# Kernel tuning notes

Measured on AMD Instinct MI355X. Metric: run time of the kernel, lower is better.

Reference implementation:

```python
import jax, jax.numpy as jnp
import numpy as np

B, S, C = 4, 8192, 256        # batch, seq len, channels
NW, WS, PSZ, D = 2048, 256, 256, 32  # words, word_size, p_size, window radius


def setup_inputs() -> dict:
    key = jax.random.key(0)
    k0, k1, k2, k3, k4 = jax.random.split(key, 5)
    q = jax.random.normal(k0, (B, S, C), jnp.float32)
    c_t = jax.random.normal(k1, (B, NW, WS), jnp.float32)
    # scale weights ~1/sqrt(fan_in) so sigmoid in predictive alignment is not saturated
    W_a = jax.random.normal(k2, (WS, C), jnp.float32) / np.sqrt(C).astype(np.float32)
    W_p = jax.random.normal(k3, (PSZ, WS), jnp.float32) / np.sqrt(WS).astype(np.float32)
    V_p = jax.random.normal(k4, (1, PSZ), jnp.float32) / np.sqrt(PSZ).astype(np.float32)
    return {"q": q, "c_t": c_t, "W_a": W_a, "W_p": W_p, "V_p": V_p}


def reference(q, c_t, W_a, W_p, V_p):
    Bq, Sq, Cq = q.shape
    # predictive alignment: p_t = S * sigmoid(V_p(tanh(W_p(c_t))))  -> [B, NW, 1]
    p_t = Sq * jax.nn.sigmoid(jnp.tanh(c_t @ W_p.T) @ V_p.T)
    # window positions s in [p-D, p+D]; torch .long() truncates (p_t > 0 so == floor)
    offs = jnp.arange(-D, D + 1)                       # [K]
    s = p_t[..., 0].astype(jnp.int32)[:, :, None] + offs  # [B, NW, K]
    # pad a leading NaN row; out-of-range indices map to it (clamp then mod)
    q_pad = jnp.concatenate([jnp.full((Bq, 1, Cq), jnp.nan, q.dtype), q], axis=1)  # [B, S+1, C]
    idx = jnp.clip(s + 1, 0, Sq + 1) % (Sq + 1)        # S+1 wraps to the NaN row (0)
    qw = jax.vmap(lambda qb, ib: qb[ib])(q_pad, idx)   # [B, NW, K, C] gathered windows
    nan_mask = jnp.isnan(qw[..., 0])                   # [B, NW, K]
    qw = jnp.where(nan_mask[..., None], 0.0, qw)       # zero invalid keys (used for output too)
    Wq = qw @ W_a.T                                    # [B, NW, K, WS]
    a_t = jnp.einsum('bwkd,bwd->bwk', Wq, c_t)         # per-window scores
    a_t = jnp.where(nan_mask, -jnp.inf, a_t)           # NaN keys -> -inf before softmax
    prob = jax.nn.softmax(a_t, axis=2)
    # Gaussian truncation around predicted position p_t
    prob = prob * jnp.exp(-2.0 * jnp.square((s.astype(q.dtype) - p_t) / D))
    out = jnp.einsum('bwk,bwkc->bwc', prob, qw)        # [B, NW, C]
    return out
```

## Files before the change

### kernel.cpp

```cpp
#include <hip/hip_runtime.h>
#include <math.h>

#define BB 4
#define S 8192
#define C 256
#define NW 2048
#define WS 256
#define PSZ 256
#define DD 32
#define KK 65
#define TOTW (BB * NW)

#define KC 64
#define LDA 68
#define NBKT 64
#define TBKT (BB * NBKT)

__global__ __launch_bounds__(256) void prep_B(const float* __restrict__ Wp,
                                              const float* __restrict__ Wa,
                                              float* __restrict__ Bp,
                                              int* __restrict__ cnt) {
    const int k = blockIdx.x;
    const int t = threadIdx.x;
    Bp[k * 512 + t] = Wp[t * WS + k];
    Bp[k * 512 + 256 + t] = Wa[k * C + t];
    if (k == 0) cnt[t] = 0;
}

__global__ __launch_bounds__(256, 4) void precomp_gemm(const float* __restrict__ ct,
                                                       const float* __restrict__ Bp,
                                                       const float* __restrict__ Vp,
                                                       float* __restrict__ ptpart,
                                                       float* __restrict__ g) {
    __shared__ __align__(16) float Al[KC][LDA];
    __shared__ __align__(16) float Bl[KC][LDA];

    const int t = threadIdx.x;
    const int bm = blockIdx.x >> 3;
    const int bn = blockIdx.x & 7;
    const int tm = t >> 4;
    const int tn = t & 15;
    const int sm = t >> 2;
    const int sf = t & 3;

    const float4* ct4 = (const float4*)ct;
    const float4* B4  = (const float4*)Bp;

    float acc[4][4] = {{0.f}};

    for (int kc = 0; kc < 256; kc += KC) {
        __syncthreads();
#pragma unroll
        for (int i = 0; i < 4; i++) {
            const float4 a = ct4[(size_t)(bm * 64 + sm) * 64 + (kc >> 2) + sf + i * 4];
            const int kl = (sf + i * 4) * 4;
            Al[kl + 0][sm] = a.x;
            Al[kl + 1][sm] = a.y;
            Al[kl + 2][sm] = a.z;
            Al[kl + 3][sm] = a.w;
        }
#pragma unroll
        for (int i = 0; i < 4; i++) {
            const float4 b = B4[(size_t)(kc + sm) * 128 + bn * 16 + sf + i * 4];
            *(float4*)&Bl[sm][(sf + i * 4) * 4] = b;
        }
        __syncthreads();

#pragma unroll 8
        for (int kk = 0; kk < KC; kk++) {
            const float4 a = *(const float4*)&Al[kk][tm * 4];
            const float4 b = *(const float4*)&Bl[kk][tn * 4];
            acc[0][0] = fmaf(a.x, b.x, acc[0][0]);
            acc[0][1] = fmaf(a.x, b.y, acc[0][1]);
            acc[0][2] = fmaf(a.x, b.z, acc[0][2]);
            acc[0][3] = fmaf(a.x, b.w, acc[0][3]);
            acc[1][0] = fmaf(a.y, b.x, acc[1][0]);
            acc[1][1] = fmaf(a.y, b.y, acc[1][1]);
            acc[1][2] = fmaf(a.y, b.z, acc[1][2]);
            acc[1][3] = fmaf(a.y, b.w, acc[1][3]);
            acc[2][0] = fmaf(a.z, b.x, acc[2][0]);
            acc[2][1] = fmaf(a.z, b.y, acc[2][1]);
            acc[2][2] = fmaf(a.z, b.z, acc[2][2]);
            acc[2][3] = fmaf(a.z, b.w, acc[2][3]);
            acc[3][0] = fmaf(a.w, b.x, acc[3][0]);
            acc[3][1] = fmaf(a.w, b.y, acc[3][1]);
            acc[3][2] = fmaf(a.w, b.z, acc[3][2]);
            acc[3][3] = fmaf(a.w, b.w, acc[3][3]);
        }
    }

    if (bn >= 4) {
        const int col = bn * 64 + tn * 4 - 256;
#pragma unroll
        for (int i = 0; i < 4; i++) {
            const int row = bm * 64 + tm * 4 + i;
            *(float4*)&g[(size_t)row * 256 + col] =
                make_float4(acc[i][0], acc[i][1], acc[i][2], acc[i][3]);
        }
    } else {
        const float4 vp4 = ((const float4*)Vp)[bn * 16 + tn];
#pragma unroll
        for (int i = 0; i < 4; i++) {
            float v = tanhf(acc[i][0]) * vp4.x;
            v = fmaf(tanhf(acc[i][1]), vp4.y, v);
            v = fmaf(tanhf(acc[i][2]), vp4.z, v);
            v = fmaf(tanhf(acc[i][3]), vp4.w, v);
#pragma unroll
            for (int off = 8; off >= 1; off >>= 1) v += __shfl_xor(v, off);
            if (tn == 0) {
                const int row = bm * 64 + tm * 4 + i;
                ptpart[row * 4 + bn] = v;
            }
        }
    }
}

__global__ __launch_bounds__(256) void pt_hist(const float* __restrict__ ptpart,
                                               float* __restrict__ pt,
                                               int* __restrict__ cnt) {
    const int wg = blockIdx.x * 256 + threadIdx.x;
    const float4 pp = ((const float4*)ptpart)[wg];
    const float x = (pp.x + pp.y) + (pp.z + pp.w);
    const float p = (float)S / (1.f + expf(-x));
    pt[wg] = p;
    const int s0 = (int)p;
    const int bkt = (wg >> 11) * NBKT + min(NBKT - 1, max(0, s0 >> 7));
    atomicAdd(&cnt[bkt], 1);
}

__global__ __launch_bounds__(256) void scan_kernel(const int* __restrict__ cnt,
                                                   int* __restrict__ offs) {
    __shared__ int sh[TBKT];
    const int t = threadIdx.x;
    const int v = cnt[t];
    sh[t] = v;
    __syncthreads();
    for (int d = 1; d < TBKT; d <<= 1) {
        const int x = (t >= d) ? sh[t - d] : 0;
        __syncthreads();
        sh[t] += x;
        __syncthreads();
    }
    offs[t] = sh[t] - v;
}

__global__ __launch_bounds__(256) void scatter_kernel(const float* __restrict__ pt,
                                                      int* __restrict__ offs,
                                                      int* __restrict__ perm) {
    const int wg = blockIdx.x * 256 + threadIdx.x;
    const int s0 = (int)pt[wg];
    const int bkt = (wg >> 11) * NBKT + min(NBKT - 1, max(0, s0 >> 7));
    const int pos = atomicAdd(&offs[bkt], 1);
    perm[pos] = wg;
}

__global__ __launch_bounds__(256) void attn(const float* __restrict__ q,
                                            const float* __restrict__ g,
                                            const float* __restrict__ pt,
                                            const int* __restrict__ perm,
                                            float* __restrict__ out) {
    const int tid = threadIdx.x;
    const int lane = tid & 63;
    const int wv = tid >> 6;
    const int bid = blockIdx.x;
    const int sb = (bid & 7) * 256 + (bid >> 3);
    const int wg = perm[sb * 4 + wv];
    const int b = wg >> 11;
    const int grp = lane >> 4;
    const int sub = lane & 15;

    const float p = pt[wg];
    const int s0 = (int)p;

    const float* grow = g + (size_t)wg * C + sub * 4;
    const float4 g0 = *(const float4*)(grow);
    const float4 g1 = *(const float4*)(grow + 64);
    const float4 g2 = *(const float4*)(grow + 128);
    const float4 g3 = *(const float4*)(grow + 192);

    const float* qb = q + (size_t)b * S * C + sub * 4;

    float e[17];
#pragma unroll
    for (int it = 0; it < 17; it++) {
        const int k = it * 4 + grp;
        const int s = s0 + k - DD;
        const bool valid = (k <= 64) && ((unsigned)s < (unsigned)S);
        const float* qr = qb + (size_t)min(max(s, 0), S - 1) * C;
        const float4 q0 = *(const float4*)(qr);
        const float4 q1 = *(const float4*)(qr + 64);
        const float4 q2 = *(const float4*)(qr + 128);
        const float4 q3 = *(const float4*)(qr + 192);

        float d0 = q0.x * g0.x, d1 = q1.x * g1.x, d2 = q2.x * g2.x, d3 = q3.x * g3.x;
        d0 = fmaf(q0.y, g0.y, d0); d1 = fmaf(q1.y, g1.y, d1);
        d2 = fmaf(q2.y, g2.y, d2); d3 = fmaf(q3.y, g3.y, d3);
        d0 = fmaf(q0.z, g0.z, d0); d1 = fmaf(q1.z, g1.z, d1);
        d2 = fmaf(q2.z, g2.z, d2); d3 = fmaf(q3.z, g3.z, d3);
        d0 = fmaf(q0.w, g0.w, d0); d1 = fmaf(q1.w, g1.w, d1);
        d2 = fmaf(q2.w, g2.w, d2); d3 = fmaf(q3.w, g3.w, d3);
        float d = (d0 + d1) + (d2 + d3);
#pragma unroll
        for (int off = 8; off >= 1; off >>= 1) d += __shfl_xor(d, off);
        e[it] = valid ? d : -3e38f;
    }

    float m = e[0];
#pragma unroll
    for (int it = 1; it < 17; it++) m = fmaxf(m, e[it]);
    float M = fmaxf(m, __shfl_xor(m, 16));
    M = fmaxf(M, __shfl_xor(M, 32));

    float den = 0.f;
#pragma unroll
    for (int it = 0; it < 17; it++) {
        e[it] = __expf(e[it] - M);
        den += e[it];
    }
    den += __shfl_xor(den, 16);
    den += __shfl_xor(den, 32);

#pragma unroll
    for (int it = 0; it < 17; it++) {
        const int s = s0 + it * 4 + grp - DD;
        const float fs = (float)s - p;
        const float tt = fs * (1.f / (float)DD);
        e[it] *= __expf(-2.f * tt * tt);
    }

    float4 a0 = {0, 0, 0, 0}, a1 = {0, 0, 0, 0}, a2 = {0, 0, 0, 0}, a3 = {0, 0, 0, 0};
#pragma unroll
    for (int it = 0; it < 17; it++) {
        const int s = s0 + it * 4 + grp - DD;
        const float* qr = qb + (size_t)min(max(s, 0), S - 1) * C;
        const float4 q0 = *(const float4*)(qr);
        const float4 q1 = *(const float4*)(qr + 64);
        const float4 q2 = *(const float4*)(qr + 128);
        const float4 q3 = *(const float4*)(qr + 192);
        const float w = e[it];
        a0.x = fmaf(w, q0.x, a0.x); a0.y = fmaf(w, q0.y, a0.y);
        a0.z = fmaf(w, q0.z, a0.z); a0.w = fmaf(w, q0.w, a0.w);
        a1.x = fmaf(w, q1.x, a1.x); a1.y = fmaf(w, q1.y, a1.y);
        a1.z = fmaf(w, q1.z, a1.z); a1.w = fmaf(w, q1.w, a1.w);
        a2.x = fmaf(w, q2.x, a2.x); a2.y = fmaf(w, q2.y, a2.y);
        a2.z = fmaf(w, q2.z, a2.z); a2.w = fmaf(w, q2.w, a2.w);
        a3.x = fmaf(w, q3.x, a3.x); a3.y = fmaf(w, q3.y, a3.y);
        a3.z = fmaf(w, q3.z, a3.z); a3.w = fmaf(w, q3.w, a3.w);
    }

#define MERGE(v) { v += __shfl_xor(v, 16); v += __shfl_xor(v, 32); }
    MERGE(a0.x) MERGE(a0.y) MERGE(a0.z) MERGE(a0.w)
    MERGE(a1.x) MERGE(a1.y) MERGE(a1.z) MERGE(a1.w)
    MERGE(a2.x) MERGE(a2.y) MERGE(a2.z) MERGE(a2.w)
    MERGE(a3.x) MERGE(a3.y) MERGE(a3.z) MERGE(a3.w)
#undef MERGE

    float4 o = a0;
    if (grp == 1) o = a1;
    else if (grp == 2) o = a2;
    else if (grp == 3) o = a3;

    const float r = 1.f / den;
    o.x *= r; o.y *= r; o.z *= r; o.w *= r;

    *(float4*)(out + (size_t)wg * C + lane * 4) = o;
}

extern "C" void kernel_launch(void* const* d_in, const int* in_sizes, int n_in,
                              void* d_out, int out_size, void* d_ws, size_t ws_size,
                              hipStream_t stream) {
    const float* q  = (const float*)d_in[0];
    const float* ct = (const float*)d_in[1];
    const float* Wa = (const float*)d_in[2];
    const float* Wp = (const float*)d_in[3];
    const float* Vp = (const float*)d_in[4];
    float* out = (float*)d_out;

    char* ws = (char*)d_ws;
    float* Bp     = (float*)ws;
    float* ptpart = (float*)(ws + 524288);
    float* pt     = (float*)(ws + 655360);
    int*   cnt    = (int*)  (ws + 688128);
    int*   offs   = (int*)  (ws + 689152);
    int*   perm   = (int*)  (ws + 690176);
    float* g      = (float*)(ws + 722944);

    prep_B<<<256, 256, 0, stream>>>(Wp, Wa, Bp, cnt);
    precomp_gemm<<<1024, 256, 0, stream>>>(ct, Bp, Vp, ptpart, g);
    pt_hist<<<TOTW / 256, 256, 0, stream>>>(ptpart, pt, cnt);
    scan_kernel<<<1, TBKT, 0, stream>>>(cnt, offs);
    scatter_kernel<<<TOTW / 256, 256, 0, stream>>>(pt, offs, perm);
    attn<<<TOTW / 4, 256, 0, stream>>>(q, g, pt, perm, out);
}
```

Before: 93.41 us.

## Split each window across four waves and keep gathered q rows in registers

```diff
diff --git a/kernel.cpp b/kernel.cpp
--- a/kernel.cpp
+++ b/kernel.cpp
@@ -154,20 +154,25 @@
     perm[pos] = wg;
 }
 
-__global__ __launch_bounds__(256) void attn(const float* __restrict__ q,
-                                            const float* __restrict__ g,
-                                            const float* __restrict__ pt,
-                                            const int* __restrict__ perm,
-                                            float* __restrict__ out) {
+__global__ __launch_bounds__(256, 3) void attn(const float* __restrict__ q,
+                                               const float* __restrict__ g,
+                                               const float* __restrict__ pt,
+                                               const int* __restrict__ perm,
+                                               float* __restrict__ out) {
+    __shared__ __align__(16) float4 accbuf[4][64];
+    __shared__ float mbuf[4], dbuf[4];
+
     const int tid = threadIdx.x;
-    const int lane = tid & 63;
+    const int l = tid & 63;
     const int wv = tid >> 6;
+    const int gw = l >> 4;
+    const int sub = l & 15;
+    const int kslot = tid >> 4;
+
     const int bid = blockIdx.x;
-    const int sb = (bid & 7) * 256 + (bid >> 3);
-    const int wg = perm[sb * 4 + wv];
+    const int sb = (bid & 7) * 1024 + (bid >> 3);
+    const int wg = perm[sb];
     const int b = wg >> 11;
-    const int grp = lane >> 4;
-    const int sub = lane & 15;
 
     const float p = pt[wg];
     const int s0 = (int)p;
@@ -180,25 +185,31 @@
 
     const float* qb = q + (size_t)b * S * C + sub * 4;
 
-    float e[17];
-#pragma unroll
-    for (int it = 0; it < 17; it++) {
-        const int k = it * 4 + grp;
+    float4 qh[5][4];
+#pragma unroll
+    for (int it = 0; it < 5; it++) {
+        const int s = s0 + it * 16 + kslot - DD;
+        const float* qr = qb + (size_t)min(max(s, 0), S - 1) * C;
+        qh[it][0] = *(const float4*)(qr);
+        qh[it][1] = *(const float4*)(qr + 64);
+        qh[it][2] = *(const float4*)(qr + 128);
+        qh[it][3] = *(const float4*)(qr + 192);
+    }
+
+    float e[5];
+#pragma unroll
+    for (int it = 0; it < 5; it++) {
+        const int k = it * 16 + kslot;
         const int s = s0 + k - DD;
         const bool valid = (k <= 64) && ((unsigned)s < (unsigned)S);
-        const float* qr = qb + (size_t)min(max(s, 0), S - 1) * C;
-        const float4 q0 = *(const float4*)(qr);
-        const float4 q1 = *(const float4*)(qr + 64);
-        const float4 q2 = *(const float4*)(qr + 128);
-        const float4 q3 = *(const float4*)(qr + 192);
-
-        float d0 = q0.x * g0.x, d1 = q1.x * g1.x, d2 = q2.x * g2.x, d3 = q3.x * g3.x;
-        d0 = fmaf(q0.y, g0.y, d0); d1 = fmaf(q1.y, g1.y, d1);
-        d2 = fmaf(q2.y, g2.y, d2); d3 = fmaf(q3.y, g3.y, d3);
-        d0 = fmaf(q0.z, g0.z, d0); d1 = fmaf(q1.z, g1.z, d1);
-        d2 = fmaf(q2.z, g2.z, d2); d3 = fmaf(q3.z, g3.z, d3);
-        d0 = fmaf(q0.w, g0.w, d0); d1 = fmaf(q1.w, g1.w, d1);
-        d2 = fmaf(q2.w, g2.w, d2); d3 = fmaf(q3.w, g3.w, d3);
+        float d0 = qh[it][0].x * g0.x, d1 = qh[it][1].x * g1.x;
+        float d2 = qh[it][2].x * g2.x, d3 = qh[it][3].x * g3.x;
+        d0 = fmaf(qh[it][0].y, g0.y, d0); d1 = fmaf(qh[it][1].y, g1.y, d1);
+        d2 = fmaf(qh[it][2].y, g2.y, d2); d3 = fmaf(qh[it][3].y, g3.y, d3);
+        d0 = fmaf(qh[it][0].z, g0.z, d0); d1 = fmaf(qh[it][1].z, g1.z, d1);
+        d2 = fmaf(qh[it][2].z, g2.z, d2); d3 = fmaf(qh[it][3].z, g3.z, d3);
+        d0 = fmaf(qh[it][0].w, g0.w, d0); d1 = fmaf(qh[it][1].w, g1.w, d1);
+        d2 = fmaf(qh[it][2].w, g2.w, d2); d3 = fmaf(qh[it][3].w, g3.w, d3);
         float d = (d0 + d1) + (d2 + d3);
 #pragma unroll
         for (int off = 8; off >= 1; off >>= 1) d += __shfl_xor(d, off);
@@ -207,45 +218,38 @@
 
     float m = e[0];
 #pragma unroll
-    for (int it = 1; it < 17; it++) m = fmaxf(m, e[it]);
-    float M = fmaxf(m, __shfl_xor(m, 16));
-    M = fmaxf(M, __shfl_xor(M, 32));
+    for (int it = 1; it < 5; it++) m = fmaxf(m, e[it]);
+    m = fmaxf(m, __shfl_xor(m, 16));
+    m = fmaxf(m, __shfl_xor(m, 32));
 
     float den = 0.f;
 #pragma unroll
-    for (int it = 0; it < 17; it++) {
-        e[it] = __expf(e[it] - M);
+    for (int it = 0; it < 5; it++) {
+        e[it] = __expf(e[it] - m);
         den += e[it];
     }
     den += __shfl_xor(den, 16);
     den += __shfl_xor(den, 32);
 
 #pragma unroll
-    for (int it = 0; it < 17; it++) {
-        const int s = s0 + it * 4 + grp - DD;
-        const float fs = (float)s - p;
+    for (int it = 0; it < 5; it++) {
+        const float fs = (float)(s0 + it * 16 + kslot - DD) - p;
         const float tt = fs * (1.f / (float)DD);
         e[it] *= __expf(-2.f * tt * tt);
     }
 
-    float4 a0 = {0, 0, 0, 0}, a1 = {0, 0, 0, 0}, a2 = {0, 0, 0, 0}, a3 = {0, 0, 0, 0};
-#pragma unroll
-    for (int it = 0; it < 17; it++) {
-        const int s = s0 + it * 4 + grp - DD;
-        const float* qr = qb + (size_t)min(max(s, 0), S - 1) * C;
-        const float4 q0 = *(const float4*)(qr);
-        const float4 q1 = *(const float4*)(qr + 64);
-        const float4 q2 = *(const float4*)(qr + 128);
-        const float4 q3 = *(const float4*)(qr + 192);
+    float4 a0 = {0,0,0,0}, a1 = {0,0,0,0}, a2 = {0,0,0,0}, a3 = {0,0,0,0};
+#pragma unroll
+    for (int it = 0; it < 5; it++) {
         const float w = e[it];
-        a0.x = fmaf(w, q0.x, a0.x); a0.y = fmaf(w, q0.y, a0.y);
-        a0.z = fmaf(w, q0.z, a0.z); a0.w = fmaf(w, q0.w, a0.w);
-        a1.x = fmaf(w, q1.x, a1.x); a1.y = fmaf(w, q1.y, a1.y);
-        a1.z = fmaf(w, q1.z, a1.z); a1.w = fmaf(w, q1.w, a1.w);
-        a2.x = fmaf(w, q2.x, a2.x); a2.y = fmaf(w, q2.y, a2.y);
-        a2.z = fmaf(w, q2.z, a2.z); a2.w = fmaf(w, q2.w, a2.w);
-        a3.x = fmaf(w, q3.x, a3.x); a3.y = fmaf(w, q3.y, a3.y);
-        a3.z = fmaf(w, q3.z, a3.z); a3.w = fmaf(w, q3.w, a3.w);
+        a0.x = fmaf(w, qh[it][0].x, a0.x); a0.y = fmaf(w, qh[it][0].y, a0.y);
+        a0.z = fmaf(w, qh[it][0].z, a0.z); a0.w = fmaf(w, qh[it][0].w, a0.w);
+        a1.x = fmaf(w, qh[it][1].x, a1.x); a1.y = fmaf(w, qh[it][1].y, a1.y);
+        a1.z = fmaf(w, qh[it][1].z, a1.z); a1.w = fmaf(w, qh[it][1].w, a1.w);
+        a2.x = fmaf(w, qh[it][2].x, a2.x); a2.y = fmaf(w, qh[it][2].y, a2.y);
+        a2.z = fmaf(w, qh[it][2].z, a2.z); a2.w = fmaf(w, qh[it][2].w, a2.w);
+        a3.x = fmaf(w, qh[it][3].x, a3.x); a3.y = fmaf(w, qh[it][3].y, a3.y);
+        a3.z = fmaf(w, qh[it][3].z, a3.z); a3.w = fmaf(w, qh[it][3].w, a3.w);
     }
 
 #define MERGE(v) { v += __shfl_xor(v, 16); v += __shfl_xor(v, 32); }
@@ -256,14 +260,32 @@
 #undef MERGE
 
     float4 o = a0;
-    if (grp == 1) o = a1;
-    else if (grp == 2) o = a2;
-    else if (grp == 3) o = a3;
-
-    const float r = 1.f / den;
-    o.x *= r; o.y *= r; o.z *= r; o.w *= r;
-
-    *(float4*)(out + (size_t)wg * C + lane * 4) = o;
+    if (gw == 1) o = a1;
+    else if (gw == 2) o = a2;
+    else if (gw == 3) o = a3;
+    accbuf[wv][l] = o;
+    if (l == 0) { mbuf[wv] = m; dbuf[wv] = den; }
+    __syncthreads();
+
+    if (tid < 64) {
+        const float M = fmaxf(fmaxf(mbuf[0], mbuf[1]), fmaxf(mbuf[2], mbuf[3]));
+        const float sc0 = __expf(mbuf[0] - M);
+        const float sc1 = __expf(mbuf[1] - M);
+        const float sc2 = __expf(mbuf[2] - M);
+        const float sc3 = __expf(mbuf[3] - M);
+        const float dtot = dbuf[0]*sc0 + dbuf[1]*sc1 + dbuf[2]*sc2 + dbuf[3]*sc3;
+        const float4 v0 = accbuf[0][tid];
+        const float4 v1 = accbuf[1][tid];
+        const float4 v2 = accbuf[2][tid];
+        const float4 v3 = accbuf[3][tid];
+        const float r = 1.f / dtot;
+        float4 oo;
+        oo.x = (v0.x*sc0 + v1.x*sc1 + v2.x*sc2 + v3.x*sc3) * r;
+        oo.y = (v0.y*sc0 + v1.y*sc1 + v2.y*sc2 + v3.y*sc3) * r;
+        oo.z = (v0.z*sc0 + v1.z*sc1 + v2.z*sc2 + v3.z*sc3) * r;
+        oo.w = (v0.w*sc0 + v1.w*sc1 + v2.w*sc2 + v3.w*sc3) * r;
+        *(float4*)(out + (size_t)wg * C + tid * 4) = oo;
+    }
 }
 
 extern "C" void kernel_launch(void* const* d_in, const int* in_sizes, int n_in,
@@ -290,5 +312,5 @@
     pt_hist<<<TOTW / 256, 256, 0, stream>>>(ptpart, pt, cnt);
     scan_kernel<<<1, TBKT, 0, stream>>>(cnt, offs);
     scatter_kernel<<<TOTW / 256, 256, 0, stream>>>(pt, offs, perm);
-    attn<<<TOTW / 4, 256, 0, stream>>>(q, g, pt, perm, out);
-}
+    attn<<<TOTW, 256, 0, stream>>>(q, g, pt, perm, out);
+}
```

After: 88.65 us. 1.05x faster.

## Fuse bucket sort into one kernel and give each window a whole block

Applied to the files above, without the earlier changes.

```diff
diff --git a/kernel.cpp b/kernel.cpp
--- a/kernel.cpp
+++ b/kernel.cpp
@@ -18,13 +18,11 @@
 
 __global__ __launch_bounds__(256) void prep_B(const float* __restrict__ Wp,
                                               const float* __restrict__ Wa,
-                                              float* __restrict__ Bp,
-                                              int* __restrict__ cnt) {
+                                              float* __restrict__ Bp) {
     const int k = blockIdx.x;
     const int t = threadIdx.x;
     Bp[k * 512 + t] = Wp[t * WS + k];
     Bp[k * 512 + 256 + t] = Wa[k * C + t];
-    if (k == 0) cnt[t] = 0;
 }
 
 __global__ __launch_bounds__(256, 4) void precomp_gemm(const float* __restrict__ ct,
@@ -115,43 +113,48 @@
     }
 }
 
-__global__ __launch_bounds__(256) void pt_hist(const float* __restrict__ ptpart,
-                                               float* __restrict__ pt,
-                                               int* __restrict__ cnt) {
-    const int wg = blockIdx.x * 256 + threadIdx.x;
-    const float4 pp = ((const float4*)ptpart)[wg];
-    const float x = (pp.x + pp.y) + (pp.z + pp.w);
-    const float p = (float)S / (1.f + expf(-x));
-    pt[wg] = p;
-    const int s0 = (int)p;
-    const int bkt = (wg >> 11) * NBKT + min(NBKT - 1, max(0, s0 >> 7));
-    atomicAdd(&cnt[bkt], 1);
-}
-
-__global__ __launch_bounds__(256) void scan_kernel(const int* __restrict__ cnt,
-                                                   int* __restrict__ offs) {
-    __shared__ int sh[TBKT];
+__global__ __launch_bounds__(256) void sort_all(const float* __restrict__ ptpart,
+                                                float* __restrict__ pt,
+                                                int* __restrict__ perm) {
+    __shared__ int hist[TBKT];
+    __shared__ int scan[TBKT];
+
     const int t = threadIdx.x;
-    const int v = cnt[t];
-    sh[t] = v;
+    hist[t] = 0;
+    __syncthreads();
+
+    int bkt[32];
+#pragma unroll
+    for (int it = 0; it < 32; it++) {
+        const int wg = it * 256 + t;
+        const float4 pp = ((const float4*)ptpart)[wg];
+        const float x = (pp.x + pp.y) + (pp.z + pp.w);
+        const float p = (float)S / (1.f + expf(-x));
+        pt[wg] = p;
+        const int s0 = (int)p;
+        bkt[it] = (wg >> 11) * NBKT + min(NBKT - 1, max(0, s0 >> 7));
+        atomicAdd(&hist[bkt[it]], 1);
+    }
+    __syncthreads();
+
+    int v = hist[t];
+    scan[t] = v;
     __syncthreads();
     for (int d = 1; d < TBKT; d <<= 1) {
-        const int x = (t >= d) ? sh[t - d] : 0;
+        const int x = (t >= d) ? scan[t - d] : 0;
         __syncthreads();
-        sh[t] += x;
+        scan[t] += x;
         __syncthreads();
     }
-    offs[t] = sh[t] - v;
-}
-
-__global__ __launch_bounds__(256) void scatter_kernel(const float* __restrict__ pt,
-                                                      int* __restrict__ offs,
-                                                      int* __restrict__ perm) {
-    const int wg = blockIdx.x * 256 + threadIdx.x;
-    const int s0 = (int)pt[wg];
-    const int bkt = (wg >> 11) * NBKT + min(NBKT - 1, max(0, s0 >> 7));
-    const int pos = atomicAdd(&offs[bkt], 1);
-    perm[pos] = wg;
+    hist[t] = scan[t] - v;
+    __syncthreads();
+
+#pragma unroll
+    for (int it = 0; it < 32; it++) {
+        const int wg = it * 256 + t;
+        const int pos = atomicAdd(&hist[bkt[it]], 1);
+        perm[pos] = wg;
+    }
 }
 
 __global__ __launch_bounds__(256) void attn(const float* __restrict__ q,
@@ -159,15 +162,19 @@
                                             const float* __restrict__ pt,
                                             const int* __restrict__ perm,
                                             float* __restrict__ out) {
+    __shared__ __align__(16) float4 pbuf[16][68];
+    __shared__ float mbuf[4], dbuf[4];
+
     const int tid = threadIdx.x;
-    const int lane = tid & 63;
+    const int l = tid & 63;
     const int wv = tid >> 6;
+    const int sub = l & 15;
+    const int kslot = tid >> 4;
+
     const int bid = blockIdx.x;
-    const int sb = (bid & 7) * 256 + (bid >> 3);
-    const int wg = perm[sb * 4 + wv];
+    const int sb = (bid & 7) * 1024 + (bid >> 3);
+    const int wg = perm[sb];
     const int b = wg >> 11;
-    const int grp = lane >> 4;
-    const int sub = lane & 15;
 
     const float p = pt[wg];
     const int s0 = (int)p;
@@ -180,10 +187,10 @@
 
     const float* qb = q + (size_t)b * S * C + sub * 4;
 
-    float e[17];
-#pragma unroll
-    for (int it = 0; it < 17; it++) {
-        const int k = it * 4 + grp;
+    float e[5];
+#pragma unroll
+    for (int it = 0; it < 5; it++) {
+        const int k = it * 16 + kslot;
         const int s = s0 + k - DD;
         const bool valid = (k <= 64) && ((unsigned)s < (unsigned)S);
         const float* qr = qb + (size_t)min(max(s, 0), S - 1) * C;
@@ -191,7 +198,6 @@
         const float4 q1 = *(const float4*)(qr + 64);
         const float4 q2 = *(const float4*)(qr + 128);
         const float4 q3 = *(const float4*)(qr + 192);
-
         float d0 = q0.x * g0.x, d1 = q1.x * g1.x, d2 = q2.x * g2.x, d3 = q3.x * g3.x;
         d0 = fmaf(q0.y, g0.y, d0); d1 = fmaf(q1.y, g1.y, d1);
         d2 = fmaf(q2.y, g2.y, d2); d3 = fmaf(q3.y, g3.y, d3);
@@ -207,31 +213,34 @@
 
     float m = e[0];
 #pragma unroll
-    for (int it = 1; it < 17; it++) m = fmaxf(m, e[it]);
-    float M = fmaxf(m, __shfl_xor(m, 16));
-    M = fmaxf(M, __shfl_xor(M, 32));
+    for (int it = 1; it < 5; it++) m = fmaxf(m, e[it]);
+    m = fmaxf(m, __shfl_xor(m, 16));
+    m = fmaxf(m, __shfl_xor(m, 32));
+    if (l == 0) mbuf[wv] = m;
+    __syncthreads();
+    const float M = fmaxf(fmaxf(mbuf[0], mbuf[1]), fmaxf(mbuf[2], mbuf[3]));
 
     float den = 0.f;
 #pragma unroll
-    for (int it = 0; it < 17; it++) {
+    for (int it = 0; it < 5; it++) {
         e[it] = __expf(e[it] - M);
         den += e[it];
     }
     den += __shfl_xor(den, 16);
     den += __shfl_xor(den, 32);
-
-#pragma unroll
-    for (int it = 0; it < 17; it++) {
-        const int s = s0 + it * 4 + grp - DD;
-        const float fs = (float)s - p;
+    if (l == 0) dbuf[wv] = den;
+
+#pragma unroll
+    for (int it = 0; it < 5; it++) {
+        const float fs = (float)(s0 + it * 16 + kslot - DD) - p;
         const float tt = fs * (1.f / (float)DD);
         e[it] *= __expf(-2.f * tt * tt);
     }
 
-    float4 a0 = {0, 0, 0, 0}, a1 = {0, 0, 0, 0}, a2 = {0, 0, 0, 0}, a3 = {0, 0, 0, 0};
-#pragma unroll
-    for (int it = 0; it < 17; it++) {
-        const int s = s0 + it * 4 + grp - DD;
+    float4 a0 = {0,0,0,0}, a1 = {0,0,0,0}, a2 = {0,0,0,0}, a3 = {0,0,0,0};
+#pragma unroll
+    for (int it = 0; it < 5; it++) {
+        const int s = s0 + it * 16 + kslot - DD;
         const float* qr = qb + (size_t)min(max(s, 0), S - 1) * C;
         const float4 q0 = *(const float4*)(qr);
         const float4 q1 = *(const float4*)(qr + 64);
@@ -248,22 +257,25 @@
         a3.z = fmaf(w, q3.z, a3.z); a3.w = fmaf(w, q3.w, a3.w);
     }
 
-#define MERGE(v) { v += __shfl_xor(v, 16); v += __shfl_xor(v, 32); }
-    MERGE(a0.x) MERGE(a0.y) MERGE(a0.z) MERGE(a0.w)
-    MERGE(a1.x) MERGE(a1.y) MERGE(a1.z) MERGE(a1.w)
-    MERGE(a2.x) MERGE(a2.y) MERGE(a2.z) MERGE(a2.w)
-    MERGE(a3.x) MERGE(a3.y) MERGE(a3.z) MERGE(a3.w)
-#undef MERGE
-
-    float4 o = a0;
-    if (grp == 1) o = a1;
-    else if (grp == 2) o = a2;
-    else if (grp == 3) o = a3;
-
-    const float r = 1.f / den;
-    o.x *= r; o.y *= r; o.z *= r; o.w *= r;
-
-    *(float4*)(out + (size_t)wg * C + lane * 4) = o;
+    pbuf[kslot][0 * 17 + sub] = a0;
+    pbuf[kslot][1 * 17 + sub] = a1;
+    pbuf[kslot][2 * 17 + sub] = a2;
+    pbuf[kslot][3 * 17 + sub] = a3;
+    __syncthreads();
+
+    if (tid < 64) {
+        const float dtot = dbuf[0] + dbuf[1] + dbuf[2] + dbuf[3];
+        const int j = tid >> 4, sb2 = tid & 15;
+        float4 s0v = {0,0,0,0};
+#pragma unroll
+        for (int ks = 0; ks < 16; ks++) {
+            const float4 v = pbuf[ks][j * 17 + sb2];
+            s0v.x += v.x; s0v.y += v.y; s0v.z += v.z; s0v.w += v.w;
+        }
+        const float r = 1.f / dtot;
+        s0v.x *= r; s0v.y *= r; s0v.z *= r; s0v.w *= r;
+        *(float4*)(out + (size_t)wg * C + tid * 4) = s0v;
+    }
 }
 
 extern "C" void kernel_launch(void* const* d_in, const int* in_sizes, int n_in,
@@ -280,15 +292,11 @@
     float* Bp     = (float*)ws;
     float* ptpart = (float*)(ws + 524288);
     float* pt     = (float*)(ws + 655360);
-    int*   cnt    = (int*)  (ws + 688128);
-    int*   offs   = (int*)  (ws + 689152);
-    int*   perm   = (int*)  (ws + 690176);
-    float* g      = (float*)(ws + 722944);
-
-    prep_B<<<256, 256, 0, stream>>>(Wp, Wa, Bp, cnt);
+    int*   perm   = (int*)  (ws + 688128);
+    float* g      = (float*)(ws + 720896);
+
+    prep_B<<<256, 256, 0, stream>>>(Wp, Wa, Bp);
     precomp_gemm<<<1024, 256, 0, stream>>>(ct, Bp, Vp, ptpart, g);
-    pt_hist<<<TOTW / 256, 256, 0, stream>>>(ptpart, pt, cnt);
-    scan_kernel<<<1, TBKT, 0, stream>>>(cnt, offs);
-    scatter_kernel<<<TOTW / 256, 256, 0, stream>>>(pt, offs, perm);
-    attn<<<TOTW / 4, 256, 0, stream>>>(q, g, pt, perm, out);
-}
+    sort_all<<<1, 256, 0, stream>>>(ptpart, pt, perm);
+    attn<<<TOTW, 256, 0, stream>>>(q, g, pt, perm, out);
+}
```

New measurement: 103.5 us. 1.11x slower.
